# Kernel optimization log

Hardware: AMD Instinct MI355X
Metric: run time of the kernel (lower is better)

The kernel has to match this reference:

```python
import jax, jax.numpy as jnp
import numpy as np

N = 50000
EPS = 1e-16


def _gat_conv(x, w, att_src, att_dst, bias, src, dst, heads, out_ch, concat):
    # x: [N, F_in]; w: [heads*out_ch, F_in]; att_*: [heads, out_ch]; bias: [heads*out_ch] or [out_ch]
    n = x.shape[0]
    xw = (x @ w.T).reshape(n, heads, out_ch)              # [N, H, C]
    a_src = jnp.einsum('nhc,hc->nh', xw, att_src)          # [N, H]
    a_dst = jnp.einsum('nhc,hc->nh', xw, att_dst)
    alpha = a_src[src] + a_dst[dst]                        # [E, H]
    alpha = jax.nn.leaky_relu(alpha, negative_slope=0.2)
    # segment softmax over destination node (every node has a self loop)
    m = jax.ops.segment_max(alpha, dst, num_segments=n)    # [N, H]
    e = jnp.exp(alpha - m[dst])
    s = jax.ops.segment_sum(e, dst, num_segments=n)        # [N, H]
    coef = e / (s[dst] + EPS)                              # [E, H]
    out = jax.ops.segment_sum(xw[src] * coef[:, :, None], dst, num_segments=n)  # [N, H, C]
    if concat:
        out = out.reshape(n, heads * out_ch)
    else:
        out = out.mean(axis=1)
    return out + bias


def setup_inputs() -> dict:
    key = jax.random.key(0)
    ks = jax.random.split(key, 8)
    F_in, H, C1, NC = 128, 2, 64, 16
    E = 1_600_000
    x = jax.random.normal(ks[0], (N, F_in), dtype=jnp.float32)
    edge_index = jax.random.randint(ks[1], (2, E), 0, N, dtype=jnp.int64)
    w1 = jax.random.normal(ks[2], (H * C1, F_in), dtype=jnp.float32) / np.sqrt(F_in)
    att_src1 = jax.random.normal(ks[3], (H, C1), dtype=jnp.float32) / np.sqrt(C1)
    att_dst1 = jax.random.normal(ks[4], (H, C1), dtype=jnp.float32) / np.sqrt(C1)
    b1 = jnp.zeros((H * C1,), dtype=jnp.float32)
    w2 = jax.random.normal(ks[5], (NC, H * C1), dtype=jnp.float32) / np.sqrt(H * C1)
    att_src2 = jax.random.normal(ks[6], (1, NC), dtype=jnp.float32) / np.sqrt(NC)
    att_dst2 = jax.random.normal(ks[7], (1, NC), dtype=jnp.float32) / np.sqrt(NC)
    b2 = jnp.zeros((NC,), dtype=jnp.float32)
    return {"x": x, "edge_index": edge_index, "w1": w1, "att_src1": att_src1,
            "att_dst1": att_dst1, "b1": b1, "w2": w2, "att_src2": att_src2,
            "att_dst2": att_dst2, "b2": b2}


def reference(x, edge_index, w1, att_src1, att_dst1, b1, w2, att_src2, att_dst2, b2):
    n = x.shape[0]
    loop = jnp.arange(n, dtype=edge_index.dtype)
    src = jnp.concatenate([edge_index[0], loop])  # PyG adds self loops by default
    dst = jnp.concatenate([edge_index[1], loop])
    h = _gat_conv(x, w1, att_src1, att_dst1, b1, src, dst, heads=2, out_ch=64, concat=True)
    h = jax.nn.relu(h)
    # dropout p=0.5 is identity in eval mode
    out = _gat_conv(h, w2, att_src2, att_dst2, b2, src, dst, heads=1, out_ch=16, concat=True)
    return out
```

## Files before the change

### kernel.cpp

```cpp
#include <hip/hip_runtime.h>
#include <hip/hip_fp16.h>


#define BSHIFT 7
#define MAXB 512
#define CAPMAX 6144
#define XS 136

using f16x8 = __attribute__((ext_vector_type(8))) _Float16;
using f16x4 = __attribute__((ext_vector_type(4))) _Float16;
using f32x4 = __attribute__((ext_vector_type(4))) float;

__device__ __forceinline__ float lrelu(float a) { return fmaxf(a, 0.2f * a); }


__global__ __launch_bounds__(256) void part_gemm1_kernel(
    const int* __restrict__ src, const int* __restrict__ dst,
    int* __restrict__ bincur, unsigned* __restrict__ binned,
    int E, int B, int CH, int CAP, int NB,
    const float* __restrict__ x, const float* __restrict__ w1,
    const float* __restrict__ as1, const float* __restrict__ ad1,
    __half* __restrict__ xw1h, float* __restrict__ asrc1,
    float* __restrict__ adst1, int N) {
  __shared__ __align__(16) char smem[(64 + 128) * XS * 2];
  int t = threadIdx.x;

  if (blockIdx.x < (unsigned)NB) {
    int* s_h = (int*)smem;
    int* s_base = s_h + MAXB;
    int* s_cur = s_base + MAXB;
    unsigned* s_pack = (unsigned*)(s_cur + MAXB);
    for (int i = t; i < B; i += 256) s_h[i] = 0;
    __syncthreads();
    int lo = blockIdx.x * CH;
    int cnt = min(CH, E - lo);
    for (int i = t; i < cnt; i += 256) {
      int d = dst[lo + i];
      int s = src[lo + i];
      atomicAdd(&s_h[d >> BSHIFT], 1);
      s_pack[i] = (unsigned)s | ((unsigned)(d & 127) << 16) |
                  ((unsigned)(d >> BSHIFT) << 23);
    }
    __syncthreads();
    for (int i = t; i < B; i += 256) {
      int c = s_h[i];
      s_base[i] = c ? (i * CAP + atomicAdd(&bincur[i], c)) : 0;
      s_cur[i] = 0;
    }
    __syncthreads();
    for (int i = t; i < cnt; i += 256) {
      unsigned e = s_pack[i];
      int b = e >> 23;
      int r = atomicAdd(&s_cur[b], 1);
      binned[s_base[b] + r] = e & 0x7FFFFFu;
    }
    return;
  }

  _Float16* lx = (_Float16*)smem;
  _Float16* lw = lx + 64 * XS;
  int n0 = (blockIdx.x - NB) * 64;

#pragma unroll
  for (int j = 0; j < 8; ++j) {
    int idx = t + 256 * j;
    int nd = idx >> 5, i4 = (idx & 31) * 4;
    int gn = n0 + nd;
    float4 v = (gn < N) ? *(const float4*)&x[(size_t)gn * 128 + i4]
                        : make_float4(0.f, 0.f, 0.f, 0.f);
    f16x4 h;
    h[0] = (_Float16)v.x; h[1] = (_Float16)v.y;
    h[2] = (_Float16)v.z; h[3] = (_Float16)v.w;
    *(f16x4*)&lx[nd * XS + i4] = h;
  }
#pragma unroll
  for (int j = 0; j < 16; ++j) {
    int idx = t + 256 * j;
    int o = idx >> 5, i4 = (idx & 31) * 4;
    float4 v = *(const float4*)&w1[(size_t)o * 128 + i4];
    f16x4 h;
    h[0] = (_Float16)v.x; h[1] = (_Float16)v.y;
    h[2] = (_Float16)v.z; h[3] = (_Float16)v.w;
    *(f16x4*)&lw[o * XS + i4] = h;
  }
  __syncthreads();

  int lane = t & 63, wv = t >> 6;
  int m16 = lane & 15, q = lane >> 4;

  f32x4 acc[8];
#pragma unroll
  for (int i = 0; i < 8; ++i) acc[i] = (f32x4){0.f, 0.f, 0.f, 0.f};

#pragma unroll
  for (int c = 0; c < 4; ++c) {
    f16x8 a = *(const f16x8*)&lx[(16 * wv + m16) * XS + c * 32 + q * 8];
#pragma unroll
    for (int tt = 0; tt < 8; ++tt) {
      f16x8 b = *(const f16x8*)&lw[(tt * 16 + m16) * XS + c * 32 + q * 8];
      acc[tt] = __builtin_amdgcn_mfma_f32_16x16x32_f16(a, b, acc[tt], 0, 0, 0);
    }
  }

#pragma unroll
  for (int tt = 0; tt < 8; ++tt) {
#pragma unroll
    for (int r = 0; r < 4; ++r) {
      lx[(16 * wv + 4 * q + r) * XS + tt * 16 + m16] = (_Float16)acc[tt][r];
    }
  }

  {
    float ps = 0.f, pd = 0.f;
    int p = q;
#pragma unroll
    for (int k = 0; k < 4; ++k) {
      f16x8 hv = *(const f16x8*)&lx[(16 * wv + m16) * XS + p * 32 + k * 8];
      float4 s0 = *(const float4*)&as1[p * 32 + k * 8];
      float4 s1 = *(const float4*)&as1[p * 32 + k * 8 + 4];
      float4 d0 = *(const float4*)&ad1[p * 32 + k * 8];
      float4 d1 = *(const float4*)&ad1[p * 32 + k * 8 + 4];
      ps += (float)hv[0] * s0.x + (float)hv[1] * s0.y + (float)hv[2] * s0.z +
            (float)hv[3] * s0.w + (float)hv[4] * s1.x + (float)hv[5] * s1.y +
            (float)hv[6] * s1.z + (float)hv[7] * s1.w;
      pd += (float)hv[0] * d0.x + (float)hv[1] * d0.y + (float)hv[2] * d0.z +
            (float)hv[3] * d0.w + (float)hv[4] * d1.x + (float)hv[5] * d1.y +
            (float)hv[6] * d1.z + (float)hv[7] * d1.w;
    }
    ps += __shfl_xor(ps, 16);
    pd += __shfl_xor(pd, 16);
    int n = n0 + 16 * wv + m16;
    if (n < N && (q == 0 || q == 2)) {
      int hh = q >> 1;
      asrc1[2 * n + hh] = ps;
      adst1[2 * n + hh] = pd;
    }
  }

#pragma unroll
  for (int i = 0; i < 4; ++i) {
    int m = q + 4 * i;
    int n = n0 + 16 * wv + m;
    if (n < N) {
      uint4 v = *(const uint4*)&lx[(16 * wv + m) * XS + m16 * 8];
      *(uint4*)&xw1h[(size_t)n * 128 + m16 * 8] = v;
    }
  }
}


__global__ __launch_bounds__(256) void bucket_build_kernel(const unsigned* __restrict__ binned,
                                                           const int* __restrict__ bincur,
                                                           int2* __restrict__ nodeseg,
                                                           unsigned short* __restrict__ csr,
                                                           int N, int CAP) {
  __shared__ int s_deg[128];
  __shared__ int s_cur[128];
  __shared__ int s_wsum;
  __shared__ unsigned s_edges[CAPMAX];
  int b = blockIdx.x;
  int lo = b * CAP, hi = lo + bincur[b];
  int cnt = hi - lo;
  int t = threadIdx.x;
  if (t < 128) s_deg[t] = 0;
  int stg = min(cnt, CAPMAX);
  for (int i = t; i < stg; i += 256) s_edges[i] = binned[lo + i];
  __syncthreads();
  for (int i = t; i < cnt; i += 256) {
    unsigned e = (i < CAPMAX) ? s_edges[i] : binned[lo + i];
    atomicAdd(&s_deg[e >> 16], 1);
  }
  __syncthreads();
  int lane = t & 63, wv = t >> 6;
  int v = (t < 128) ? s_deg[t] : 0;
  int incl = v;
#pragma unroll
  for (int off = 1; off < 64; off <<= 1) {
    int u = __shfl_up(incl, off);
    if (lane >= off) incl += u;
  }
  if (t == 63) s_wsum = incl;
  __syncthreads();
  int excl = incl - v + ((wv == 1) ? s_wsum : 0);
  if (t < 128) {
    int node = (b << BSHIFT) + t;
    if (node < N) nodeseg[node] = make_int2(lo + excl, lo + excl + v);
    s_cur[t] = lo + excl;
  }
  __syncthreads();
  for (int i = t; i < cnt; i += 256) {
    unsigned e = (i < CAPMAX) ? s_edges[i] : binned[lo + i];
    int p = atomicAdd(&s_cur[e >> 16], 1);
    csr[p] = (unsigned short)(e & 0xFFFFu);
  }
}


__global__ __launch_bounds__(256) void agg1_kernel(const __half* __restrict__ xw1h,
                                                   const float* __restrict__ asrc1,
                                                   const float* __restrict__ adst1,
                                                   const float* __restrict__ b1,
                                                   const float* __restrict__ w2,
                                                   const float* __restrict__ as2,
                                                   const float* __restrict__ ad2,
                                                   const unsigned short* __restrict__ csr,
                                                   const int2* __restrict__ nodeseg,
                                                   __half* __restrict__ xw2h,
                                                   float* __restrict__ asrc2,
                                                   float* __restrict__ adst2, int N) {
  __shared__ int s_off[4][64];
  __shared__ float2 s_w[4][64];
  int lane = threadIdx.x & 63, wv = threadIdx.x >> 6;
  int d = blockIdx.x * 4 + wv;
  if (d >= N) return;
  int c8 = lane & 15;
  int row = lane >> 4;
  int head = c8 >> 3;
  int2 seg = nodeseg[d];
  int e0 = seg.x, e1 = seg.y;
  float2 asv = *(const float2*)&asrc1[2 * d];
  float2 adv = *(const float2*)&adst1[2 * d];
  float wself = __expf(lrelu(head ? (asv.y + adv.y) : (asv.x + adv.x)));

  const char* xb = (const char*)xw1h + 16 * c8;

  float a[8];
  float sum = 0.f;
#pragma unroll
  for (int k = 0; k < 8; ++k) a[k] = 0.f;
  if (row == 0) {
    uint4 r = *(const uint4*)(xb + ((size_t)d << 8));
    const __half2* hp = (const __half2*)&r;
#pragma unroll
    for (int k = 0; k < 4; ++k) {
      float2 v = __half22float2(hp[k]);
      a[2 * k] = wself * v.x;
      a[2 * k + 1] = wself * v.y;
    }
    sum = wself;
  }

  for (int base = e0; base < e1; base += 64) {
    int cnt = min(64, e1 - base);
    if (lane < cnt) {
      int s = (int)csr[base + lane];
      float2 aa = *(const float2*)&asrc1[2 * s];
      s_off[wv][lane] = s << 8;
      float2 w;
      w.x = __expf(lrelu(aa.x + adv.x));
      w.y = __expf(lrelu(aa.y + adv.y));
      s_w[wv][lane] = w;
    }
    int j = 0;
    for (; j + 7 < cnt; j += 8) {
      int oA = s_off[wv][j + row];
      int oB = s_off[wv][j + 4 + row];
      float wA = ((const float*)&s_w[wv][j + row])[head];
      float wB = ((const float*)&s_w[wv][j + 4 + row])[head];
      uint4 rA = *(const uint4*)(xb + oA);
      uint4 rB = *(const uint4*)(xb + oB);
      const __half2* hA = (const __half2*)&rA;
      const __half2* hB = (const __half2*)&rB;
#pragma unroll
      for (int k = 0; k < 4; ++k) {
        float2 vA = __half22float2(hA[k]);
        float2 vB = __half22float2(hB[k]);
        a[2 * k] += wA * vA.x + wB * vB.x;
        a[2 * k + 1] += wA * vA.y + wB * vB.y;
      }
      sum += wA + wB;
    }
    for (; j < cnt; j += 4) {
      if (row < cnt - j) {
        int oA = s_off[wv][j + row];
        float wA = ((const float*)&s_w[wv][j + row])[head];
        uint4 rA = *(const uint4*)(xb + oA);
        const __half2* hA = (const __half2*)&rA;
#pragma unroll
        for (int k = 0; k < 4; ++k) {
          float2 vA = __half22float2(hA[k]);
          a[2 * k] += wA * vA.x;
          a[2 * k + 1] += wA * vA.y;
        }
        sum += wA;
      }
    }
  }

#pragma unroll
  for (int k = 0; k < 8; ++k) {
    a[k] += __shfl_xor(a[k], 16);
    a[k] += __shfl_xor(a[k], 32);
  }
  sum += __shfl_xor(sum, 16);
  sum += __shfl_xor(sum, 32);

  float inv = 1.f / (sum + 1e-16f);
  float4 blo = *(const float4*)&b1[8 * c8];
  float4 bhi = *(const float4*)&b1[8 * c8 + 4];
  float h[8];
  h[0] = fmaxf(a[0] * inv + blo.x, 0.f);
  h[1] = fmaxf(a[1] * inv + blo.y, 0.f);
  h[2] = fmaxf(a[2] * inv + blo.z, 0.f);
  h[3] = fmaxf(a[3] * inv + blo.w, 0.f);
  h[4] = fmaxf(a[4] * inv + bhi.x, 0.f);
  h[5] = fmaxf(a[5] * inv + bhi.y, 0.f);
  h[6] = fmaxf(a[6] * inv + bhi.z, 0.f);
  h[7] = fmaxf(a[7] * inv + bhi.w, 0.f);

  float p[4];
#pragma unroll
  for (int cc = 0; cc < 4; ++cc) {
    const float4 wlo = *(const float4*)&w2[(row * 4 + cc) * 128 + 8 * c8];
    const float4 whi = *(const float4*)&w2[(row * 4 + cc) * 128 + 8 * c8 + 4];
    p[cc] = h[0] * wlo.x + h[1] * wlo.y + h[2] * wlo.z + h[3] * wlo.w +
            h[4] * whi.x + h[5] * whi.y + h[6] * whi.z + h[7] * whi.w;
#pragma unroll
    for (int k = 1; k < 16; k <<= 1) p[cc] += __shfl_xor(p[cc], k);
  }
  float qs = 0.f, qd = 0.f;
#pragma unroll
  for (int cc = 0; cc < 4; ++cc) {
    qs += p[cc] * as2[row * 4 + cc];
    qd += p[cc] * ad2[row * 4 + cc];
  }
  qs += __shfl_xor(qs, 16);
  qs += __shfl_xor(qs, 32);
  qd += __shfl_xor(qd, 16);
  qd += __shfl_xor(qd, 32);
  if (lane == 0) {
    asrc2[d] = qs;
    adst2[d] = qd;
  }
  if (c8 == 0) {
    union {
      __half hh[4];
      uint2 u;
    } pk;
#pragma unroll
    for (int cc = 0; cc < 4; ++cc) pk.hh[cc] = __float2half(p[cc]);
    *(uint2*)&xw2h[(size_t)d * 16 + row * 4] = pk.u;
  }
}


__global__ __launch_bounds__(256) void agg2_kernel(const __half* __restrict__ xw2h,
                                                   const float* __restrict__ asrc2,
                                                   const float* __restrict__ adst2,
                                                   const float* __restrict__ b2,
                                                   const unsigned short* __restrict__ csr,
                                                   const int2* __restrict__ nodeseg,
                                                   float* __restrict__ out, int N) {
  __shared__ int s_off[4][64];
  __shared__ float s_w[4][64];
  int lane = threadIdx.x & 63, wv = threadIdx.x >> 6;
  int d = blockIdx.x * 4 + wv;
  if (d >= N) return;
  int c2 = lane & 7;
  int row = lane >> 3;
  int2 seg = nodeseg[d];
  int e0 = seg.x, e1 = seg.y;
  float advd = adst2[d];
  float wself = __expf(lrelu(asrc2[d] + advd));
  const char* xb = (const char*)xw2h + 4 * c2;

  float a0 = 0.f, a1 = 0.f, sum = 0.f;
  if (row == 0) {
    float2 v = __half22float2(*(const __half2*)(xb + (size_t)d * 32));
    a0 = wself * v.x;
    a1 = wself * v.y;
    sum = wself;
  }
  for (int base = e0; base < e1; base += 64) {
    int cnt = min(64, e1 - base);
    if (lane < cnt) {
      int s = (int)csr[base + lane];
      s_off[wv][lane] = s << 5;
      s_w[wv][lane] = __expf(lrelu(asrc2[s] + advd));
    }
    int j = 0;
    for (; j + 15 < cnt; j += 16) {
      int o0 = s_off[wv][j + row];
      int o1 = s_off[wv][j + 8 + row];
      float w0 = s_w[wv][j + row];
      float w1 = s_w[wv][j + 8 + row];
      float2 v0 = __half22float2(*(const __half2*)(xb + o0));
      float2 v1 = __half22float2(*(const __half2*)(xb + o1));
      a0 += w0 * v0.x + w1 * v1.x;
      a1 += w0 * v0.y + w1 * v1.y;
      sum += w0 + w1;
    }
    for (; j + 7 < cnt; j += 8) {
      int o0 = s_off[wv][j + row];
      float w0 = s_w[wv][j + row];
      float2 v0 = __half22float2(*(const __half2*)(xb + o0));
      a0 += w0 * v0.x;
      a1 += w0 * v0.y;
      sum += w0;
    }
    if (row < cnt - j) {
      int o0 = s_off[wv][j + row];
      float w0 = s_w[wv][j + row];
      float2 v0 = __half22float2(*(const __half2*)(xb + o0));
      a0 += w0 * v0.x;
      a1 += w0 * v0.y;
      sum += w0;
    }
  }
#pragma unroll
  for (int k = 8; k < 64; k <<= 1) {
    a0 += __shfl_xor(a0, k);
    a1 += __shfl_xor(a1, k);
    sum += __shfl_xor(sum, k);
  }
  if (lane < 8) {
    float inv = 1.f / (sum + 1e-16f);
    float2 r;
    r.x = a0 * inv + b2[2 * c2];
    r.y = a1 * inv + b2[2 * c2 + 1];
    *(float2*)&out[(size_t)d * 16 + 2 * c2] = r;
  }
}


extern "C" void kernel_launch(void* const* d_in, const int* in_sizes, int n_in,
                              void* d_out, int out_size, void* d_ws, size_t ws_size,
                              hipStream_t stream) {
  const float* x = (const float*)d_in[0];
  const int* ei = (const int*)d_in[1];
  const float* w1 = (const float*)d_in[2];
  const float* as1 = (const float*)d_in[3];
  const float* ad1 = (const float*)d_in[4];
  const float* b1 = (const float*)d_in[5];
  const float* w2 = (const float*)d_in[6];
  const float* as2 = (const float*)d_in[7];
  const float* ad2 = (const float*)d_in[8];
  const float* b2 = (const float*)d_in[9];
  float* out = (float*)d_out;

  int N = in_sizes[0] / 128;
  int E = in_sizes[1] / 2;
  const int* srcp = ei;
  const int* dstp = ei + E;

  int B = (N + (1 << BSHIFT) - 1) >> BSHIFT;
  int mean = (E + B - 1) / B;
  int CAP = (mean + mean / 4 + 512 + 255) & ~255;
  const int NB = 256;
  int CH = (E + NB - 1) / NB;
  int GB = (N + 63) / 64;

  char* p = (char*)d_ws;
  auto alloc = [&](size_t bytes) -> void* {
    void* r = (void*)p;
    p += (bytes + 255) & ~(size_t)255;
    return r;
  };
  __half* xw1h = (__half*)alloc((size_t)N * 128 * 2);
  float* asrc1 = (float*)alloc((size_t)N * 2 * 4);
  float* adst1 = (float*)alloc((size_t)N * 2 * 4);
  __half* xw2h = (__half*)alloc((size_t)N * 16 * 2);
  float* asrc2 = (float*)alloc((size_t)N * 4);
  float* adst2 = (float*)alloc((size_t)N * 4);
  int2* nodeseg = (int2*)alloc((size_t)N * 8);
  unsigned short* csr = (unsigned short*)alloc((size_t)B * CAP * 2);
  unsigned* binned = (unsigned*)alloc((size_t)B * CAP * 4);
  int* bincur = (int*)alloc((size_t)B * 4);

  hipMemsetAsync(bincur, 0, (size_t)B * 4, stream);
  part_gemm1_kernel<<<NB + GB, 256, 0, stream>>>(srcp, dstp, bincur, binned,
                                                 E, B, CH, CAP, NB,
                                                 x, w1, as1, ad1, xw1h, asrc1, adst1, N);
  bucket_build_kernel<<<B, 256, 0, stream>>>(binned, bincur, nodeseg, csr, N, CAP);
  agg1_kernel<<<(N + 3) / 4, 256, 0, stream>>>(xw1h, asrc1, adst1, b1, w2, as2, ad2,
                                               csr, nodeseg, xw2h, asrc2, adst2, N);
  agg2_kernel<<<(N + 3) / 4, 256, 0, stream>>>(xw2h, asrc2, adst2, b2, csr, nodeseg, out, N);
}
```

Baseline: 209.5 us.

## Split layer-1 aggregation into column slices and move layer-2 GEMM to MFMA kernel

The fused agg1 kernel is split in two. A column-sliced aggregation kernel has each block handle a 32-column slice of the 128 features, so each gather fetches 4 bytes per lane instead of 16. The intent is that blocks working on the same slice share a smaller working set that stays in cache. The layer-2 projection and its attention dot-products move to a separate kernel that uses MFMA f16 instructions on 64-node tiles. The cost is that the CSR walk and edge-weight exps are repeated four times, and an extra fp16 hidden buffer must be written and read back.

```diff
diff --git a/kernel.cpp b/kernel.cpp
--- a/kernel.cpp
+++ b/kernel.cpp
@@ -196,150 +196,146 @@
 }
 
 
-__global__ __launch_bounds__(256) void agg1_kernel(const __half* __restrict__ xw1h,
-                                                   const float* __restrict__ asrc1,
-                                                   const float* __restrict__ adst1,
-                                                   const float* __restrict__ b1,
-                                                   const float* __restrict__ w2,
-                                                   const float* __restrict__ as2,
-                                                   const float* __restrict__ ad2,
-                                                   const unsigned short* __restrict__ csr,
-                                                   const int2* __restrict__ nodeseg,
-                                                   __half* __restrict__ xw2h,
-                                                   float* __restrict__ asrc2,
-                                                   float* __restrict__ adst2, int N) {
+__global__ __launch_bounds__(256) void agg1s_kernel(const __half* __restrict__ xw1h,
+                                                    const float* __restrict__ asrc1,
+                                                    const float* __restrict__ adst1,
+                                                    const float* __restrict__ b1,
+                                                    const unsigned short* __restrict__ csr,
+                                                    const int2* __restrict__ nodeseg,
+                                                    __half* __restrict__ hout, int N) {
   __shared__ int s_off[4][64];
-  __shared__ float2 s_w[4][64];
+  __shared__ float s_w[4][64];
   int lane = threadIdx.x & 63, wv = threadIdx.x >> 6;
-  int d = blockIdx.x * 4 + wv;
-  if (d >= N) return;
-  int c8 = lane & 15;
+  int slice = blockIdx.x & 3;
+  int g = blockIdx.x >> 2;
+  int hs = slice >> 1;
+  int c16 = lane & 15;
   int row = lane >> 4;
-  int head = c8 >> 3;
-  int2 seg = nodeseg[d];
-  int e0 = seg.x, e1 = seg.y;
-  float2 asv = *(const float2*)&asrc1[2 * d];
-  float2 adv = *(const float2*)&adst1[2 * d];
-  float wself = __expf(lrelu(head ? (asv.y + adv.y) : (asv.x + adv.x)));
-
-  const char* xb = (const char*)xw1h + 16 * c8;
-
-  float a[8];
-  float sum = 0.f;
-#pragma unroll
-  for (int k = 0; k < 8; ++k) a[k] = 0.f;
-  if (row == 0) {
-    uint4 r = *(const uint4*)(xb + ((size_t)d << 8));
-    const __half2* hp = (const __half2*)&r;
-#pragma unroll
-    for (int k = 0; k < 4; ++k) {
-      float2 v = __half22float2(hp[k]);
-      a[2 * k] = wself * v.x;
-      a[2 * k + 1] = wself * v.y;
-    }
-    sum = wself;
-  }
-
-  for (int base = e0; base < e1; base += 64) {
-    int cnt = min(64, e1 - base);
-    if (lane < cnt) {
-      int s = (int)csr[base + lane];
-      float2 aa = *(const float2*)&asrc1[2 * s];
-      s_off[wv][lane] = s << 8;
-      float2 w;
-      w.x = __expf(lrelu(aa.x + adv.x));
-      w.y = __expf(lrelu(aa.y + adv.y));
-      s_w[wv][lane] = w;
-    }
-    int j = 0;
-    for (; j + 7 < cnt; j += 8) {
-      int oA = s_off[wv][j + row];
-      int oB = s_off[wv][j + 4 + row];
-      float wA = ((const float*)&s_w[wv][j + row])[head];
-      float wB = ((const float*)&s_w[wv][j + 4 + row])[head];
-      uint4 rA = *(const uint4*)(xb + oA);
-      uint4 rB = *(const uint4*)(xb + oB);
-      const __half2* hA = (const __half2*)&rA;
-      const __half2* hB = (const __half2*)&rB;
-#pragma unroll
-      for (int k = 0; k < 4; ++k) {
-        float2 vA = __half22float2(hA[k]);
-        float2 vB = __half22float2(hB[k]);
-        a[2 * k] += wA * vA.x + wB * vB.x;
-        a[2 * k + 1] += wA * vA.y + wB * vB.y;
+  const char* xb = (const char*)xw1h + slice * 64 + c16 * 4;
+  float2 bv = *(const float2*)&b1[slice * 32 + c16 * 2];
+
+#pragma unroll
+  for (int u = 0; u < 2; ++u) {
+    int d = g * 8 + wv * 2 + u;
+    if (d >= N) return;
+    int2 seg = nodeseg[d];
+    int e0 = seg.x, e1 = seg.y;
+    float adv = adst1[2 * d + hs];
+    float wself = __expf(lrelu(asrc1[2 * d + hs] + adv));
+
+    float a0 = 0.f, a1 = 0.f, sum = 0.f;
+    if (row == 0) {
+      float2 v = __half22float2(*(const __half2*)(xb + ((size_t)d << 8)));
+      a0 = wself * v.x;
+      a1 = wself * v.y;
+      sum = wself;
+    }
+
+    for (int base = e0; base < e1; base += 64) {
+      int cnt = min(64, e1 - base);
+      if (lane < cnt) {
+        int s = (int)csr[base + lane];
+        s_off[wv][lane] = s << 8;
+        s_w[wv][lane] = __expf(lrelu(asrc1[2 * s + hs] + adv));
       }
-      sum += wA + wB;
-    }
-    for (; j < cnt; j += 4) {
-      if (row < cnt - j) {
+      int j = 0;
+      for (; j + 7 < cnt; j += 8) {
         int oA = s_off[wv][j + row];
-        float wA = ((const float*)&s_w[wv][j + row])[head];
-        uint4 rA = *(const uint4*)(xb + oA);
-        const __half2* hA = (const __half2*)&rA;
-#pragma unroll
-        for (int k = 0; k < 4; ++k) {
-          float2 vA = __half22float2(hA[k]);
-          a[2 * k] += wA * vA.x;
-          a[2 * k + 1] += wA * vA.y;
+        int oB = s_off[wv][j + 4 + row];
+        float wA = s_w[wv][j + row];
+        float wB = s_w[wv][j + 4 + row];
+        float2 vA = __half22float2(*(const __half2*)(xb + oA));
+        float2 vB = __half22float2(*(const __half2*)(xb + oB));
+        a0 += wA * vA.x + wB * vB.x;
+        a1 += wA * vA.y + wB * vB.y;
+        sum += wA + wB;
+      }
+      for (; j < cnt; j += 4) {
+        if (row < cnt - j) {
+          int oA = s_off[wv][j + row];
+          float wA = s_w[wv][j + row];
+          float2 vA = __half22float2(*(const __half2*)(xb + oA));
+          a0 += wA * vA.x;
+          a1 += wA * vA.y;
+          sum += wA;
         }
-        sum += wA;
       }
     }
-  }
-
-#pragma unroll
-  for (int k = 0; k < 8; ++k) {
-    a[k] += __shfl_xor(a[k], 16);
-    a[k] += __shfl_xor(a[k], 32);
-  }
-  sum += __shfl_xor(sum, 16);
-  sum += __shfl_xor(sum, 32);
-
-  float inv = 1.f / (sum + 1e-16f);
-  float4 blo = *(const float4*)&b1[8 * c8];
-  float4 bhi = *(const float4*)&b1[8 * c8 + 4];
-  float h[8];
-  h[0] = fmaxf(a[0] * inv + blo.x, 0.f);
-  h[1] = fmaxf(a[1] * inv + blo.y, 0.f);
-  h[2] = fmaxf(a[2] * inv + blo.z, 0.f);
-  h[3] = fmaxf(a[3] * inv + blo.w, 0.f);
-  h[4] = fmaxf(a[4] * inv + bhi.x, 0.f);
-  h[5] = fmaxf(a[5] * inv + bhi.y, 0.f);
-  h[6] = fmaxf(a[6] * inv + bhi.z, 0.f);
-  h[7] = fmaxf(a[7] * inv + bhi.w, 0.f);
-
-  float p[4];
-#pragma unroll
-  for (int cc = 0; cc < 4; ++cc) {
-    const float4 wlo = *(const float4*)&w2[(row * 4 + cc) * 128 + 8 * c8];
-    const float4 whi = *(const float4*)&w2[(row * 4 + cc) * 128 + 8 * c8 + 4];
-    p[cc] = h[0] * wlo.x + h[1] * wlo.y + h[2] * wlo.z + h[3] * wlo.w +
-            h[4] * whi.x + h[5] * whi.y + h[6] * whi.z + h[7] * whi.w;
-#pragma unroll
-    for (int k = 1; k < 16; k <<= 1) p[cc] += __shfl_xor(p[cc], k);
-  }
-  float qs = 0.f, qd = 0.f;
-#pragma unroll
-  for (int cc = 0; cc < 4; ++cc) {
-    qs += p[cc] * as2[row * 4 + cc];
-    qd += p[cc] * ad2[row * 4 + cc];
-  }
-  qs += __shfl_xor(qs, 16);
-  qs += __shfl_xor(qs, 32);
-  qd += __shfl_xor(qd, 16);
-  qd += __shfl_xor(qd, 32);
-  if (lane == 0) {
-    asrc2[d] = qs;
-    adst2[d] = qd;
-  }
-  if (c8 == 0) {
-    union {
-      __half hh[4];
-      uint2 u;
-    } pk;
-#pragma unroll
-    for (int cc = 0; cc < 4; ++cc) pk.hh[cc] = __float2half(p[cc]);
-    *(uint2*)&xw2h[(size_t)d * 16 + row * 4] = pk.u;
+
+    a0 += __shfl_xor(a0, 16);
+    a0 += __shfl_xor(a0, 32);
+    a1 += __shfl_xor(a1, 16);
+    a1 += __shfl_xor(a1, 32);
+    sum += __shfl_xor(sum, 16);
+    sum += __shfl_xor(sum, 32);
+
+    if (row == 0) {
+      float inv = 1.f / (sum + 1e-16f);
+      __half2 hv;
+      hv.x = __float2half(fmaxf(a0 * inv + bv.x, 0.f));
+      hv.y = __float2half(fmaxf(a1 * inv + bv.y, 0.f));
+      *(__half2*)((char*)hout + ((size_t)d << 8) + slice * 64 + c16 * 4) = hv;
+    }
+  }
+}
+
+
+__global__ __launch_bounds__(256) void gemm2h_kernel(const __half* __restrict__ hbuf,
+                                                     const float* __restrict__ w2,
+                                                     const float* __restrict__ as2,
+                                                     const float* __restrict__ ad2,
+                                                     __half* __restrict__ xw2h,
+                                                     float* __restrict__ asrc2,
+                                                     float* __restrict__ adst2, int N) {
+  __shared__ __align__(16) _Float16 lw[16 * XS];
+  __shared__ __align__(16) _Float16 lh[4][16 * XS];
+  int t = threadIdx.x;
+  int n0 = blockIdx.x * 64;
+#pragma unroll
+  for (int j = 0; j < 2; ++j) {
+    int idx = t + 256 * j;
+    int o = idx >> 5, i4 = (idx & 31) * 4;
+    float4 v = *(const float4*)&w2[o * 128 + i4];
+    f16x4 hv;
+    hv[0] = (_Float16)v.x; hv[1] = (_Float16)v.y;
+    hv[2] = (_Float16)v.z; hv[3] = (_Float16)v.w;
+    *(f16x4*)&lw[o * XS + i4] = hv;
+  }
+#pragma unroll
+  for (int j = 0; j < 4; ++j) {
+    int idx = t + 256 * j;
+    int nd = idx >> 4, i8 = (idx & 15) * 8;
+    int gn = n0 + nd;
+    uint4 v = (gn < N) ? *(const uint4*)&hbuf[(size_t)gn * 128 + i8]
+                       : make_uint4(0, 0, 0, 0);
+    *(uint4*)&lh[nd >> 4][(nd & 15) * XS + i8] = v;
+  }
+  __syncthreads();
+
+  int lane = t & 63, wv = t >> 6;
+  int m16 = lane & 15, q = lane >> 4;
+  f32x4 acc = (f32x4){0.f, 0.f, 0.f, 0.f};
+#pragma unroll
+  for (int c = 0; c < 4; ++c) {
+    f16x8 a = *(const f16x8*)&lh[wv][m16 * XS + c * 32 + q * 8];
+    f16x8 b = *(const f16x8*)&lw[m16 * XS + c * 32 + q * 8];
+    acc = __builtin_amdgcn_mfma_f32_16x16x32_f16(a, b, acc, 0, 0, 0);
+  }
+  float a2v = as2[m16], d2v = ad2[m16];
+#pragma unroll
+  for (int r = 0; r < 4; ++r) {
+    int n = n0 + wv * 16 + 4 * q + r;
+    if (n < N) xw2h[(size_t)n * 16 + m16] = __float2half(acc[r]);
+    float ps = acc[r] * a2v, pd = acc[r] * d2v;
+#pragma unroll
+    for (int k = 1; k < 16; k <<= 1) {
+      ps += __shfl_xor(ps, k);
+      pd += __shfl_xor(pd, k);
+    }
+    if (m16 == 0 && n < N) {
+      asrc2[n] = ps;
+      adst2[n] = pd;
+    }
   }
 }
 
@@ -449,6 +445,7 @@
   const int NB = 256;
   int CH = (E + NB - 1) / NB;
   int GB = (N + 63) / 64;
+  int NG = (N + 7) / 8;
 
   char* p = (char*)d_ws;
   auto alloc = [&](size_t bytes) -> void* {
@@ -457,6 +454,7 @@
     return r;
   };
   __half* xw1h = (__half*)alloc((size_t)N * 128 * 2);
+  __half* hbuf = (__half*)alloc((size_t)N * 128 * 2);
   float* asrc1 = (float*)alloc((size_t)N * 2 * 4);
   float* adst1 = (float*)alloc((size_t)N * 2 * 4);
   __half* xw2h = (__half*)alloc((size_t)N * 16 * 2);
@@ -472,7 +470,8 @@
                                                  E, B, CH, CAP, NB,
                                                  x, w1, as1, ad1, xw1h, asrc1, adst1, N);
   bucket_build_kernel<<<B, 256, 0, stream>>>(binned, bincur, nodeseg, csr, N, CAP);
-  agg1_kernel<<<(N + 3) / 4, 256, 0, stream>>>(xw1h, asrc1, adst1, b1, w2, as2, ad2,
-                                               csr, nodeseg, xw2h, asrc2, adst2, N);
+  agg1s_kernel<<<4 * NG, 256, 0, stream>>>(xw1h, asrc1, adst1, b1, csr, nodeseg, hbuf, N);
+  gemm2h_kernel<<<(N + 63) / 64, 256, 0, stream>>>(hbuf, w2, as2, ad2,
+                                                   xw2h, asrc2, adst2, N);
   agg2_kernel<<<(N + 3) / 4, 256, 0, stream>>>(xw2h, asrc2, adst2, b2, csr, nodeseg, out, N);
 }
```

Measured after the change: 255.1 us. +21.8%, slower.
